# Kernel tuning notes

Measured on AMD Instinct MI355X. Metric: run time of the kernel, lower is better.

## Reference

```python
import jax, jax.numpy as jnp
import numpy as np


def setup_inputs() -> dict:
    key = jax.random.key(0)
    kq, kk, kw, kv = jax.random.split(key, 4)
    B, T, Dq, Dk, A = 32, 4096, 512, 512, 512
    q = jax.random.normal(kq, (B, Dq), dtype=jnp.float32)
    k = jax.random.normal(kk, (B, T, Dk), dtype=jnp.float32)
    # Dense kernel over concat([q, k]) last dim -> attention_size (TruncatedNormal 0.02)
    W = jax.random.truncated_normal(kw, -2.0, 2.0, (Dq + Dk, A), dtype=jnp.float32) * 0.02
    b = jnp.zeros((A,), dtype=jnp.float32)
    # VarianceScaling(scale=2.0, 'normal') over fan_in=A
    v = jax.random.normal(kv, (A,), dtype=jnp.float32) * jnp.sqrt(2.0 / A)
    return {"q": q, "k": k, "W": W, "b": b, "v": v}


def reference(q, k, W, b, v):
    # Original: tile q over T, concat with k, Dense(tanh), dot with v.
    # Equivalent (same math) without materializing the [B,T,Dq+Dk] concat:
    # split W into Wq (rows for q part) and Wk (rows for k part).
    Dq = q.shape[-1]
    Wq, Wk = W[:Dq], W[Dq:]
    qp = q @ Wq                                  # [B, A]
    kp = jnp.einsum('btd,da->bta', k, Wk)        # [B, T, A]
    out = jnp.tanh(qp[:, None, :] + kp + b)      # [B, T, A]
    score = jnp.einsum('bta,a->bt', out, v)      # [B, T]
    return score
```

## Files before the change

kernel.cpp:

```cpp
#include <hip/hip_runtime.h>
#include <hip/hip_bf16.h>
#include <stdint.h>

#define DQ 512
#define DK 512
#define NA 512
#define TT 4096
#define NBATCH 32
#define M_TOTAL (NBATCH * TT)

#define BM 64
#define BK 32
#define KITERS (DK / BK)

typedef __attribute__((ext_vector_type(8))) short bf16x8;
typedef __attribute__((ext_vector_type(4))) float f32x4;

__device__ __forceinline__ void gll16(const void* g, void* l) {
  __builtin_amdgcn_global_load_lds(
      (const __attribute__((address_space(1))) uint32_t*)g,
      (__attribute__((address_space(3))) uint32_t*)l, 16, 0, 0);
}

__device__ __forceinline__ uint32_t pack2bf16(float a, float b) {
  uint32_t ua = __float_as_uint(a) + 0x8000u;
  uint32_t ub = __float_as_uint(b) + 0x8000u;
  return __builtin_amdgcn_perm(ub, ua, 0x07060302);
}

__device__ __forceinline__ float fast_tanh(float x) {
  float e = __expf(2.0f * x);
  return 1.0f - 2.0f * __builtin_amdgcn_rcpf(e + 1.0f);
}

__global__ void prep_kernel(const float* __restrict__ W,
                            uint16_t* __restrict__ WkT) {
  __shared__ uint16_t T[64][65];
  const int tid = threadIdx.x;
  const int d0 = (blockIdx.x & 7) * 64;
  const int a0 = (blockIdx.x >> 3) * 64;
#pragma unroll
  for (int j = 0; j < 16; ++j) {
    int dd = j * 4 + (tid >> 6);
    int aa = tid & 63;
    uint32_t u = __float_as_uint(W[(size_t)(DQ + d0 + dd) * NA + a0 + aa]) + 0x8000u;
    T[dd][aa] = (uint16_t)(u >> 16);
  }
  __syncthreads();
#pragma unroll
  for (int j = 0; j < 8; ++j) {
    int aa = j * 8 + (tid >> 5);
    int dp = (tid & 31) * 2;
    uint32_t val = (uint32_t)T[dp][aa] | ((uint32_t)T[dp + 1][aa] << 16);
    *(uint32_t*)(WkT + (size_t)(a0 + aa) * DK + d0 + dp) = val;
  }
}

__global__ void qpb_kernel(const float* __restrict__ q,
                           const float* __restrict__ W,
                           const float* __restrict__ bias,
                           float* __restrict__ qpb) {
  int b = blockIdx.x >> 3;
  int a = (blockIdx.x & 7) * 64 + threadIdx.x;
  const float* qr = q + b * DQ;
  float acc = bias[a];
#pragma unroll 8
  for (int d = 0; d < DQ; ++d)
    acc = fmaf(qr[d], W[(size_t)d * NA + a], acc);
  qpb[b * NA + a] = acc;
}

__global__ __launch_bounds__(512, 4)
void score_kernel(const float* __restrict__ Kmat,
                  const uint16_t* __restrict__ WkT,
                  const float* __restrict__ qpb,
                  const float* __restrict__ v,
                  float* __restrict__ out) {
  __shared__ __align__(16) uint16_t As[BM * BK];
  __shared__ __align__(16) uint16_t Bs[NA * BK];
  __shared__ float part[8][BM];

  const int tid  = threadIdx.x;
  const int lane = tid & 63;
  const int w    = tid >> 6;
  const int r16  = lane & 15;
  const int quad = lane >> 4;
  const int m_tile = blockIdx.x;

  const float* Ag = Kmat + (size_t)m_tile * BM * DK;

  f32x4 acc[4][4];
#pragma unroll
  for (int i = 0; i < 4; ++i)
#pragma unroll
    for (int j = 0; j < 4; ++j) {
      f32x4 z = {0.f, 0.f, 0.f, 0.f};
      acc[i][j] = z;
    }

  const int arow = tid >> 3;
  const int akp  = (tid & 7) * 4;
  const float* Asrc = Ag + (size_t)arow * DK + akp;
  uint16_t* Adst = As + arow * BK + akp;

  float4 c = *(const float4*)(Asrc);

  for (int it = 0; it < KITERS; ++it) {
    const int kk = it * BK;

    __syncthreads();

#pragma unroll
    for (int j = 0; j < 4; ++j) {
      const int g0 = j * 512 + w * 64;
      const int g  = g0 + lane;
      const uint16_t* src = WkT + (size_t)(g >> 2) * DK + kk + (g & 3) * 8;
      gll16((const void*)src, (void*)((char*)Bs + (size_t)g0 * 16));
    }

    uint2 p;
    p.x = pack2bf16(c.x, c.y);
    p.y = pack2bf16(c.z, c.w);
    *(uint2*)Adst = p;

    __syncthreads();

    if (it + 1 < KITERS) c = *(const float4*)(Asrc + kk + BK);

    const bf16x8* Av = (const bf16x8*)As;
    const bf16x8* Bv = (const bf16x8*)Bs;
    bf16x8 af[4], bfr[4];
#pragma unroll
    for (int ms = 0; ms < 4; ++ms)
      af[ms] = Av[(ms * 16 + r16) * 4 + quad];
#pragma unroll
    for (int ns = 0; ns < 4; ++ns)
      bfr[ns] = Bv[(w * 64 + ns * 16 + r16) * 4 + quad];
#pragma unroll
    for (int ms = 0; ms < 4; ++ms)
#pragma unroll
      for (int ns = 0; ns < 4; ++ns)
        acc[ms][ns] = __builtin_amdgcn_mfma_f32_16x16x32_bf16(
            af[ms], bfr[ns], acc[ms][ns], 0, 0, 0);
  }

  const size_t row0 = (size_t)m_tile * BM;
  const int b_idx = m_tile >> 6;

  float vv[4], qv[4];
#pragma unroll
  for (int ns = 0; ns < 4; ++ns) {
    int a = w * 64 + ns * 16 + r16;
    vv[ns] = v[a];
    qv[ns] = qpb[b_idx * NA + a];
  }

#pragma unroll
  for (int ms = 0; ms < 4; ++ms) {
#pragma unroll
    for (int reg = 0; reg < 4; ++reg) {
      float s = 0.f;
#pragma unroll
      for (int ns = 0; ns < 4; ++ns) {
        float x = acc[ms][ns][reg] + qv[ns];
        s = fmaf(fast_tanh(x), vv[ns], s);
      }
      s += __shfl_xor(s, 1);
      s += __shfl_xor(s, 2);
      s += __shfl_xor(s, 4);
      s += __shfl_xor(s, 8);
      if (r16 == 0) part[w][ms * 16 + quad * 4 + reg] = s;
    }
  }
  __syncthreads();
  if (tid < BM) {
    float s = 0.f;
#pragma unroll
    for (int ww = 0; ww < 8; ++ww) s += part[ww][tid];
    out[row0 + tid] = s;
  }
}

extern "C" void kernel_launch(void* const* d_in, const int* in_sizes, int n_in,
                              void* d_out, int out_size, void* d_ws, size_t ws_size,
                              hipStream_t stream) {
  const float* q = (const float*)d_in[0];
  const float* k = (const float*)d_in[1];
  const float* W = (const float*)d_in[2];
  const float* b = (const float*)d_in[3];
  const float* v = (const float*)d_in[4];
  float* out = (float*)d_out;

  float* qpb = (float*)d_ws;
  uint16_t* WkT = (uint16_t*)((char*)d_ws + 65536);

  prep_kernel<<<64, 256, 0, stream>>>(W, WkT);
  qpb_kernel<<<256, 64, 0, stream>>>(q, W, b, qpb);
  score_kernel<<<M_TOTAL / BM, 512, 0, stream>>>(k, WkT, qpb, v, out);
}
```

Measured before the change: 447.1 us.

## Double-buffer score GEMM LDS, swizzle tiles, retile WkT, merge prep kernels

Double-buffers the A and B LDS tiles so the next K-slice is loaded while the current one feeds MFMA, which removes one barrier per iteration. It also applies an XOR swizzle to the LDS layouts to reduce bank conflicts, and re-lays out the transposed Wk weight into contiguous K-slab tiles so each slice is one coalesced region. The two prep kernels are merged into a single launch to cut launch overhead. Doubling the LDS footprint (about 72KB per block) may lower occupancy below the launch_bounds target of 4 blocks per CU.

```diff
diff --git a/kernel.cpp b/kernel.cpp
--- a/kernel.cpp
+++ b/kernel.cpp
@@ -34,50 +34,53 @@
 }
 
 __global__ void prep_kernel(const float* __restrict__ W,
-                            uint16_t* __restrict__ WkT) {
-  __shared__ uint16_t T[64][65];
+                            const float* __restrict__ q,
+                            const float* __restrict__ bias,
+                            uint16_t* __restrict__ WkTt,
+                            float* __restrict__ qpb) {
   const int tid = threadIdx.x;
-  const int d0 = (blockIdx.x & 7) * 64;
-  const int a0 = (blockIdx.x >> 3) * 64;
-#pragma unroll
-  for (int j = 0; j < 16; ++j) {
-    int dd = j * 4 + (tid >> 6);
-    int aa = tid & 63;
-    uint32_t u = __float_as_uint(W[(size_t)(DQ + d0 + dd) * NA + a0 + aa]) + 0x8000u;
-    T[dd][aa] = (uint16_t)(u >> 16);
-  }
-  __syncthreads();
-#pragma unroll
-  for (int j = 0; j < 8; ++j) {
-    int aa = j * 8 + (tid >> 5);
-    int dp = (tid & 31) * 2;
-    uint32_t val = (uint32_t)T[dp][aa] | ((uint32_t)T[dp + 1][aa] << 16);
-    *(uint32_t*)(WkT + (size_t)(a0 + aa) * DK + d0 + dp) = val;
-  }
-}
-
-__global__ void qpb_kernel(const float* __restrict__ q,
-                           const float* __restrict__ W,
-                           const float* __restrict__ bias,
-                           float* __restrict__ qpb) {
-  int b = blockIdx.x >> 3;
-  int a = (blockIdx.x & 7) * 64 + threadIdx.x;
-  const float* qr = q + b * DQ;
-  float acc = bias[a];
+  if (blockIdx.x < 64) {
+    __shared__ uint16_t T[64][65];
+    const int d0 = (blockIdx.x & 7) * 64;
+    const int a0 = (blockIdx.x >> 3) * 64;
+#pragma unroll
+    for (int j = 0; j < 16; ++j) {
+      int dd = j * 4 + (tid >> 6);
+      int aa = tid & 63;
+      uint32_t u = __float_as_uint(W[(size_t)(DQ + d0 + dd) * NA + a0 + aa]) + 0x8000u;
+      T[dd][aa] = (uint16_t)(u >> 16);
+    }
+    __syncthreads();
+#pragma unroll
+    for (int j = 0; j < 8; ++j) {
+      int aa = j * 8 + (tid >> 5);
+      int n  = a0 + aa;
+      int dp = (tid & 31) * 2;
+      int d  = d0 + dp;
+      uint32_t val = (uint32_t)T[dp][aa] | ((uint32_t)T[dp + 1][aa] << 16);
+      *(uint32_t*)(WkTt + (size_t)(d >> 5) * 16384 + n * 32 + (d & 31)) = val;
+    }
+  } else {
+    const int bb = blockIdx.x - 64;
+    const int b  = bb >> 1;
+    const int a  = (bb & 1) * 256 + tid;
+    const float* qr = q + b * DQ;
+    float acc = bias[a];
 #pragma unroll 8
-  for (int d = 0; d < DQ; ++d)
-    acc = fmaf(qr[d], W[(size_t)d * NA + a], acc);
-  qpb[b * NA + a] = acc;
+    for (int d = 0; d < DQ; ++d)
+      acc = fmaf(qr[d], W[(size_t)d * NA + a], acc);
+    qpb[b * NA + a] = acc;
+  }
 }
 
 __global__ __launch_bounds__(512, 4)
 void score_kernel(const float* __restrict__ Kmat,
-                  const uint16_t* __restrict__ WkT,
+                  const uint16_t* __restrict__ WkTt,
                   const float* __restrict__ qpb,
                   const float* __restrict__ v,
                   float* __restrict__ out) {
-  __shared__ __align__(16) uint16_t As[BM * BK];
-  __shared__ __align__(16) uint16_t Bs[NA * BK];
+  __shared__ __align__(16) uint16_t As[2][BM * BK];
+  __shared__ __align__(16) uint16_t Bs[2][NA * BK];
   __shared__ float part[8][BM];
 
   const int tid  = threadIdx.x;
@@ -86,6 +89,7 @@
   const int r16  = lane & 15;
   const int quad = lane >> 4;
   const int m_tile = blockIdx.x;
+  const int sw = quad ^ ((r16 >> 1) & 3);
 
   const float* Ag = Kmat + (size_t)m_tile * BM * DK;
 
@@ -98,44 +102,63 @@
       acc[i][j] = z;
     }
 
+  const uint16_t* bsrc[4];
+#pragma unroll
+  for (int j = 0; j < 4; ++j) {
+    int s   = j * 512 + w * 64 + lane;
+    int n   = s >> 2;
+    int ksl = s & 3;
+    int ks  = ksl ^ ((n >> 1) & 3);
+    bsrc[j] = WkTt + n * 32 + ks * 8;
+  }
+  const int bdst_off[4] = { (0 * 512 + w * 64) * 16, (1 * 512 + w * 64) * 16,
+                            (2 * 512 + w * 64) * 16, (3 * 512 + w * 64) * 16 };
+
   const int arow = tid >> 3;
   const int akp  = (tid & 7) * 4;
   const float* Asrc = Ag + (size_t)arow * DK + akp;
-  uint16_t* Adst = As + arow * BK + akp;
-
-  float4 c = *(const float4*)(Asrc);
-
+  const int As_off = arow * 64 + ((akp >> 3) ^ ((arow >> 1) & 3)) * 16 + (akp & 7) * 2;
+
+#pragma unroll
+  for (int j = 0; j < 4; ++j) {
+    gll16((const void*)bsrc[j], (void*)((char*)Bs[0] + bdst_off[j]));
+    bsrc[j] += 16384;
+  }
+  {
+    float4 c0 = *(const float4*)(Asrc);
+    uint2 p;
+    p.x = pack2bf16(c0.x, c0.y);
+    p.y = pack2bf16(c0.z, c0.w);
+    *(uint2*)((char*)As[0] + As_off) = p;
+  }
+  float4 c = *(const float4*)(Asrc + BK);
+
+#pragma unroll 2
   for (int it = 0; it < KITERS; ++it) {
-    const int kk = it * BK;
+    const int cur = it & 1, nxt = cur ^ 1;
 
     __syncthreads();
 
-#pragma unroll
-    for (int j = 0; j < 4; ++j) {
-      const int g0 = j * 512 + w * 64;
-      const int g  = g0 + lane;
-      const uint16_t* src = WkT + (size_t)(g >> 2) * DK + kk + (g & 3) * 8;
-      gll16((const void*)src, (void*)((char*)Bs + (size_t)g0 * 16));
-    }
-
-    uint2 p;
-    p.x = pack2bf16(c.x, c.y);
-    p.y = pack2bf16(c.z, c.w);
-    *(uint2*)Adst = p;
-
-    __syncthreads();
-
-    if (it + 1 < KITERS) c = *(const float4*)(Asrc + kk + BK);
-
-    const bf16x8* Av = (const bf16x8*)As;
-    const bf16x8* Bv = (const bf16x8*)Bs;
+    if (it + 1 < KITERS) {
+#pragma unroll
+      for (int j = 0; j < 4; ++j) {
+        gll16((const void*)bsrc[j], (void*)((char*)Bs[nxt] + bdst_off[j]));
+        bsrc[j] += 16384;
+      }
+      uint2 p;
+      p.x = pack2bf16(c.x, c.y);
+      p.y = pack2bf16(c.z, c.w);
+      *(uint2*)((char*)As[nxt] + As_off) = p;
+      if (it + 2 < KITERS) c = *(const float4*)(Asrc + (it + 2) * BK);
+    }
+
     bf16x8 af[4], bfr[4];
 #pragma unroll
     for (int ms = 0; ms < 4; ++ms)
-      af[ms] = Av[(ms * 16 + r16) * 4 + quad];
+      af[ms] = *(const bf16x8*)((char*)As[cur] + (ms * 16 + r16) * 64 + sw * 16);
 #pragma unroll
     for (int ns = 0; ns < 4; ++ns)
-      bfr[ns] = Bv[(w * 64 + ns * 16 + r16) * 4 + quad];
+      bfr[ns] = *(const bf16x8*)((char*)Bs[cur] + (w * 64 + ns * 16 + r16) * 64 + sw * 16);
 #pragma unroll
     for (int ms = 0; ms < 4; ++ms)
 #pragma unroll
@@ -192,9 +215,8 @@
   float* out = (float*)d_out;
 
   float* qpb = (float*)d_ws;
-  uint16_t* WkT = (uint16_t*)((char*)d_ws + 65536);
-
-  prep_kernel<<<64, 256, 0, stream>>>(W, WkT);
-  qpb_kernel<<<256, 64, 0, stream>>>(q, W, b, qpb);
-  score_kernel<<<M_TOTAL / BM, 512, 0, stream>>>(k, WkT, qpb, v, out);
-}
+  uint16_t* WkTt = (uint16_t*)((char*)d_ws + 65536);
+
+  prep_kernel<<<128, 256, 0, stream>>>(W, q, b, WkTt, qpb);
+  score_kernel<<<M_TOTAL / BM, 512, 0, stream>>>(k, WkTt, qpb, v, out);
+}
```

After: 436.7 us. 1.02x faster.
